# Kernel tuning notes

Hardware: AMD Instinct MI355X
Metric: run time of the kernel (lower is better)

Reference implementation:

```python
import jax, jax.numpy as jnp
import numpy as np

N_GRAM = 3
N_HEAD = 8


def setup_inputs() -> dict:
    key = jax.random.key(0)
    ks = jax.random.split(key, 8)
    V, E, H, H2, C, B, L = 50000, 512, 512, 512, 10, 64, 512
    def rn(k, shape, scale):
        return jax.random.normal(k, shape, jnp.float32) * jnp.float32(scale)
    return {
        "x": jax.random.randint(ks[0], (B, L), 0, V),
        "emb": rn(ks[1], (V, E), 0.02),
        "Wq": rn(ks[2], (H, E), 1.0 / np.sqrt(H)),
        "Wx": rn(ks[3], (E, 3 * H), 1.0 / np.sqrt(E)),
        "Wh": rn(ks[4], (H, 3 * H), 1.0 / np.sqrt(H)),
        "bx": jnp.zeros((3 * H,), jnp.float32),
        "bh": jnp.zeros((3 * H,), jnp.float32),
        "W1": rn(ks[5], (H, H2), 1.0 / np.sqrt(H)),
        "b1": jnp.zeros((H2,), jnp.float32),
        "W2": rn(ks[6], (H2, C), 1.0 / np.sqrt(H2)),
        "b2": jnp.zeros((C,), jnp.float32),
    }


def _gru_ngram_attn(xe, Wq, Wx, Wh, bx, bh):
    # xe: [B, L, E] embedded sequence
    B, L, E = xe.shape
    g, nh = N_GRAM, N_HEAD
    hd = E // nh
    H = Wh.shape[0]
    scale = jnp.float32(1.0 / np.sqrt(hd))
    xpad = jnp.pad(xe, ((0, 0), (g - 1, 0), (0, 0)))
    win = jnp.stack([xpad[:, i:i + L] for i in range(g)], axis=2)  # [B,L,g,E]
    win_t = jnp.transpose(win, (1, 0, 2, 3))  # [L,B,g,E] for scan
    h0 = jnp.zeros((B, H), xe.dtype)

    def step(h, w):
        # multi-head dot attention: query from prev hidden, keys/values = n-gram window
        q = (h @ Wq).reshape(B, nh, hd)          # [B,nh,hd]
        k = w.reshape(B, g, nh, hd)              # [B,g,nh,hd]
        scores = jnp.einsum('bnd,bgnd->bng', q, k) * scale
        a = jax.nn.softmax(scores, axis=-1)      # over window positions
        ctx = jnp.einsum('bng,bgnd->bnd', a, k).reshape(B, E)
        # GRU cell with attended context as input
        gx = ctx @ Wx + bx
        gh = h @ Wh + bh
        xr, xz, xn = jnp.split(gx, 3, axis=-1)
        hr, hz, hn = jnp.split(gh, 3, axis=-1)
        r = jax.nn.sigmoid(xr + hr)
        z = jax.nn.sigmoid(xz + hz)
        n = jnp.tanh(xn + r * hn)
        hnew = (1.0 - z) * n + z * h
        return hnew, hnew

    _, hs = jax.lax.scan(step, h0, win_t)  # [L,B,H]
    return hs


def reference(x, emb, Wq, Wx, Wh, bx, bh, W1, b1, W2, b2):
    xe = emb[x]  # [B,L,E]
    hs = _gru_ngram_attn(xe, Wq, Wx, Wh, bx, bh)  # [L,B,H]
    pooled = jax.nn.relu(hs.sum(axis=0))          # sum over seq, then relu
    out = pooled @ W1 + b1                        # fc1 path (H != embed not needed; H is GRU out)
    out = out @ W2 + b2                           # [B,C]
    return out
```

## Files before the change

kernel.cpp:

```cpp
#include <hip/hip_runtime.h>
#include <hip/hip_fp16.h>

typedef __attribute__((ext_vector_type(2))) _Float16 half2v;
typedef __attribute__((ext_vector_type(2))) __fp16   fp16x2;

#define SEQ     512
#define THREADS 512

#define WQ_OFF   0
#define WX_OFF   (64*512)
#define WH_OFF   (64*512 + 64*1536)
#define SYNC_OFF 3670016

__device__ inline unsigned int pack2f16(float a, float b) {
    fp16x2 p = __builtin_amdgcn_cvt_pkrtz(a, b);
    return __builtin_bit_cast(unsigned int, p);
}
__device__ inline float fdot2u(unsigned int a, unsigned int b, float acc) {
    return __builtin_amdgcn_fdot2(__builtin_bit_cast(half2v, a),
                                  __builtin_bit_cast(half2v, b), acc, false);
}
__device__ inline float dot4(uint4 h, uint4 w, float acc) {
    acc = fdot2u(h.x, w.x, acc); acc = fdot2u(h.y, w.y, acc);
    acc = fdot2u(h.z, w.z, acc); acc = fdot2u(h.w, w.w, acc);
    return acc;
}
__device__ inline float fsigmoid(float x) { return 1.f / (1.f + __expf(-x)); }
__device__ inline float ftanhf(float x) {
    float e = __expf(-2.f * fabsf(x));
    float t = (1.f - e) / (1.f + e);
    return copysignf(t, x);
}

__device__ inline void vmem_fence() { asm volatile("s_waitcnt vmcnt(0)" ::: "memory"); }
__device__ inline unsigned a_ld(unsigned* p) {
    return __hip_atomic_load(p, __ATOMIC_RELAXED, __HIP_MEMORY_SCOPE_AGENT);
}
__device__ inline void a_st(unsigned* p, unsigned v) {
    __hip_atomic_store(p, v, __ATOMIC_RELAXED, __HIP_MEMORY_SCOPE_AGENT);
}
__device__ inline float a_ldf(float* p) {
    return __hip_atomic_load(p, __ATOMIC_RELAXED, __HIP_MEMORY_SCOPE_AGENT);
}
__device__ inline void a_stf(float* p, float v) {
    __hip_atomic_store(p, v, __ATOMIC_RELAXED, __HIP_MEMORY_SCOPE_AGENT);
}

__global__ __launch_bounds__(256)
void pack_weights(const float* __restrict__ Wq,
                  const float* __restrict__ Wx,
                  const float* __restrict__ Wh,
                  uint4* __restrict__ ws) {
    int tid = blockIdx.x * blockDim.x + threadIdx.x;
    const float* src; uint4* dst; int C, idx;
    if (tid < 64 * 512)                  { src = Wq; dst = ws;          C = 512;  idx = tid; }
    else if (tid < 64 * 512 + 64 * 1536) { src = Wx; dst = ws + WX_OFF; C = 1536; idx = tid - 64 * 512; }
    else                                 { src = Wh; dst = ws + WH_OFF; C = 1536; idx = tid - (64 * 512 + 64 * 1536); }
    int m4 = idx / C;
    int c  = idx - m4 * C;
    const float* s = src + (size_t)(m4 * 8) * C + c;
    uint4 o;
    o.x = pack2f16(s[0 * (size_t)C], s[1 * (size_t)C]);
    o.y = pack2f16(s[2 * (size_t)C], s[3 * (size_t)C]);
    o.z = pack2f16(s[4 * (size_t)C], s[5 * (size_t)C]);
    o.w = pack2f16(s[6 * (size_t)C], s[7 * (size_t)C]);
    dst[idx] = o;
}

__global__ __launch_bounds__(THREADS)
void gru_scan(const int* __restrict__ xtok, const float* __restrict__ emb,
              const uint4* __restrict__ wsp, const float* __restrict__ bx,
              const float* __restrict__ bh, const float* __restrict__ W1,
              const float* __restrict__ b1, const float* __restrict__ W2,
              const float* __restrict__ b2, float* __restrict__ out)
{
    const int blk  = blockIdx.x;
    const int gid  = blk & 7;
    const int bid  = blk >> 3;
    const int tid  = threadIdx.x;
    const int lane = tid & 63;
    const int wid  = tid >> 6;
    const int colsub = lane & 7;
    const int bp     = (lane >> 3) & 3;
    const int chsub  = lane >> 5;

    char* sync = (char*)wsp + SYNC_OFF;
    unsigned int* flagS = (unsigned int*)sync;
    unsigned int* flagH = (unsigned int*)(sync + 1024);
    unsigned int* Hbuf  = (unsigned int*)(sync + 2048);
    float* Pbuf         = (float*)(sync + 133120);
    float* pooled_g     = (float*)(sync + 182272);
    float* fc1_g        = (float*)(sync + 313344);

    __shared__ uint4 lds_W [64][65];
    __shared__ uint4 lds_Wx[64][49];
    __shared__ uint4 lds_h [8][66];
    __shared__ uint4 lds_ctx[8][66];
    __shared__ float red[8][64][9];
    __shared__ float sum[64][9];
    __shared__ float a_lds[8][8][3];

    for (int i = tid; i < 64 * 64; i += THREADS) {
        int ch = i >> 6, cl = i & 63;
        uint4 v;
        if (cl < 16) v = wsp[WQ_OFF + ch * 512 + bid * 16 + cl];
        else { int g = (cl - 16) >> 4, c = (cl - 16) & 15;
               v = wsp[WH_OFF + ch * 1536 + g * 512 + bid * 16 + c]; }
        lds_W[ch][cl] = v;
    }
    for (int i = tid; i < 64 * 48; i += THREADS) {
        int ch = i / 48, cl = i - ch * 48;
        int g = cl >> 4, c = cl & 15;
        lds_Wx[ch][cl] = wsp[WX_OFF + ch * 1536 + g * 512 + bid * 16 + c];
    }

    float bxr = 0, bxz = 0, bxn = 0, bhr = 0, bhz = 0, bhn = 0;
    if (tid < 128) {
        int c = tid >> 3;
        int cg = bid * 16 + c;
        bxr = bx[cg]; bxz = bx[512 + cg]; bxn = bx[1024 + cg];
        bhr = bh[cg]; bhz = bh[512 + cg]; bhn = bh[1024 + cg];
    }
    float hprev = 0.f, pooledv = 0.f;
    __syncthreads();

    for (int t = 0; t < SEQ; ++t) {
        const int par = t & 1;

        const int b  = wid;
        const int gb = gid * 8 + b;
        int tk0 = (t >= 2) ? xtok[gb * SEQ + t - 2] : -1;
        int tk1 = (t >= 1) ? xtok[gb * SEQ + t - 1] : -1;
        int tk2 = xtok[gb * SEQ + t];
        float4 e0a = {0,0,0,0}, e0b = {0,0,0,0};
        float4 e1a = {0,0,0,0}, e1b = {0,0,0,0};
        float4 e2a, e2b;
        if (tk0 >= 0) { const float4* p = (const float4*)(emb + (size_t)tk0 * 512 + lane * 8); e0a = p[0]; e0b = p[1]; }
        if (tk1 >= 0) { const float4* p = (const float4*)(emb + (size_t)tk1 * 512 + lane * 8); e1a = p[0]; e1b = p[1]; }
        { const float4* p = (const float4*)(emb + (size_t)tk2 * 512 + lane * 8); e2a = p[0]; e2b = p[1]; }

        float winv[16];
        int b3 = 0, g3 = 0, trow = -1;
        if (wid == 0 && lane < 24) {
            b3 = lane / 3; g3 = lane - b3 * 3;
            trow = t - 2 + g3;
            int tok = (trow >= 0) ? xtok[(gid * 8 + b3) * SEQ + trow] : -1;
            if (tok >= 0) {
                const float* er = emb + (size_t)tok * 512 + bid * 16;
                #pragma unroll
                for (int d = 0; d < 16; ++d) winv[d] = er[d];
            } else {
                #pragma unroll
                for (int d = 0; d < 16; ++d) winv[d] = 0.f;
            }
        }

        if (wid == 0) {
            bool done = lane >= 32;
            while (!__all(done)) {
                if (!done) done = (a_ld(&flagH[gid * 32 + lane]) >= (unsigned)t);
                if (!__all(done)) __builtin_amdgcn_s_sleep(1);
            }
        }
        __syncthreads();

        {
            unsigned* hsrc = Hbuf + (size_t)(par ^ 1) * 16384;
            for (int i = tid; i < 8 * 64; i += THREADS) {
                int bb = i >> 6, ch = i & 63;
                unsigned* s = hsrc + (gid * 8 + bb) * 256 + ch * 4;
                uint4 v;
                v.x = a_ld(s); v.y = a_ld(s + 1); v.z = a_ld(s + 2); v.w = a_ld(s + 3);
                lds_h[bb][ch] = v;
            }
        }
        __syncthreads();

        {
            float aq0 = 0, aq1 = 0, aq2 = 0, aq3 = 0;
            int ch0 = wid * 8 + chsub * 4;
            #pragma unroll
            for (int i = 0; i < 4; ++i) {
                int ch = ch0 + i;
                uint4 h0 = lds_h[bp][ch], h1 = lds_h[bp + 4][ch];
                uint4 w0 = lds_W[ch][colsub], w1 = lds_W[ch][colsub + 8];
                aq0 = dot4(h0, w0, aq0); aq1 = dot4(h0, w1, aq1);
                aq2 = dot4(h1, w0, aq2); aq3 = dot4(h1, w1, aq3);
            }
            aq0 += __shfl_xor(aq0, 32); aq1 += __shfl_xor(aq1, 32);
            aq2 += __shfl_xor(aq2, 32); aq3 += __shfl_xor(aq3, 32);
            if (chsub == 0) {
                red[wid][colsub][bp]       = aq0; red[wid][colsub + 8][bp]     = aq1;
                red[wid][colsub][bp + 4]   = aq2; red[wid][colsub + 8][bp + 4] = aq3;
            }
        }
        __syncthreads();

        if (wid == 0 && lane < 24) {
            float s = 0.f;
            if (trow >= 0) {
                #pragma unroll
                for (int d = 0; d < 16; ++d) {
                    float q = red[0][d][b3];
                    #pragma unroll
                    for (int k = 1; k < 8; ++k) q += red[k][d][b3];
                    s += winv[d] * q;
                }
            }
            a_stf(&Pbuf[(size_t)((par * 8 + gid) * 32 + bid) * 24 + b3 * 3 + g3], s);
        }
        if (wid == 0) {
            vmem_fence();
            if (lane == 0) a_st(&flagS[gid * 32 + bid], (unsigned)(t + 1));
        }

        {
            float ag[12];
            #pragma unroll
            for (int i = 0; i < 12; ++i) ag[i] = 0.f;
            int ch0 = wid * 8 + chsub * 4;
            #pragma unroll
            for (int i = 0; i < 4; ++i) {
                int ch = ch0 + i;
                uint4 h0 = lds_h[bp][ch], h1 = lds_h[bp + 4][ch];
                #pragma unroll
                for (int j = 0; j < 6; ++j) {
                    uint4 w = lds_W[ch][16 + colsub + 8 * j];
                    ag[j]     = dot4(h0, w, ag[j]);
                    ag[6 + j] = dot4(h1, w, ag[6 + j]);
                }
            }
            #pragma unroll
            for (int i = 0; i < 12; ++i) ag[i] += __shfl_xor(ag[i], 32);
            if (chsub == 0) {
                #pragma unroll
                for (int j = 0; j < 6; ++j) {
                    red[wid][16 + colsub + 8 * j][bp]     = ag[j];
                    red[wid][16 + colsub + 8 * j][bp + 4] = ag[6 + j];
                }
            }
        }
        __syncthreads();

        if (tid >= 64 && tid < 448) {
            int idx = tid - 64;
            int col = 16 + (idx >> 3), bb = idx & 7;
            float s = red[0][col][bb];
            #pragma unroll
            for (int k = 1; k < 8; ++k) s += red[k][col][bb];
            sum[col][bb] = s;
        }
        if (wid == 0) {
            bool done = lane >= 32;
            while (!__all(done)) {
                if (!done) done = (a_ld(&flagS[gid * 32 + lane]) >= (unsigned)(t + 1));
                if (!__all(done)) __builtin_amdgcn_s_sleep(1);
            }
        }
        __syncthreads();

        if (tid < 64) {
            int bb = tid >> 3, n = tid & 7;
            float* pb = Pbuf + (size_t)(par * 8 + gid) * 32 * 24;
            float sc0 = 0, sc1 = 0, sc2 = 0;
            #pragma unroll
            for (int j = 0; j < 4; ++j) {
                float* pj = pb + (n * 4 + j) * 24 + bb * 3;
                sc0 += a_ldf(pj); sc1 += a_ldf(pj + 1); sc2 += a_ldf(pj + 2);
            }
            sc0 *= 0.125f; sc1 *= 0.125f; sc2 *= 0.125f;
            float mx = fmaxf(sc0, fmaxf(sc1, sc2));
            float e0 = __expf(sc0 - mx), e1 = __expf(sc1 - mx), e2 = __expf(sc2 - mx);
            float inv = 1.f / (e0 + e1 + e2);
            a_lds[bb][n][0] = e0 * inv; a_lds[bb][n][1] = e1 * inv; a_lds[bb][n][2] = e2 * inv;
        }
        __syncthreads();

        {
            int head = lane >> 3;
            float a0 = a_lds[b][head][0], a1 = a_lds[b][head][1], a2 = a_lds[b][head][2];
            float c0 = a0 * e0a.x + a1 * e1a.x + a2 * e2a.x;
            float c1 = a0 * e0a.y + a1 * e1a.y + a2 * e2a.y;
            float c2 = a0 * e0a.z + a1 * e1a.z + a2 * e2a.z;
            float c3 = a0 * e0a.w + a1 * e1a.w + a2 * e2a.w;
            float c4 = a0 * e0b.x + a1 * e1b.x + a2 * e2b.x;
            float c5 = a0 * e0b.y + a1 * e1b.y + a2 * e2b.y;
            float c6 = a0 * e0b.z + a1 * e1b.z + a2 * e2b.z;
            float c7 = a0 * e0b.w + a1 * e1b.w + a2 * e2b.w;
            uint4 pk;
            pk.x = pack2f16(c0, c1); pk.y = pack2f16(c2, c3);
            pk.z = pack2f16(c4, c5); pk.w = pack2f16(c6, c7);
            lds_ctx[b][lane] = pk;
        }
        __syncthreads();

        {
            float acx[12];
            #pragma unroll
            for (int i = 0; i < 12; ++i) acx[i] = 0.f;
            int ch0 = wid * 8 + chsub * 4;
            #pragma unroll
            for (int i = 0; i < 4; ++i) {
                int ch = ch0 + i;
                uint4 c0 = lds_ctx[bp][ch];
                uint4 c1 = lds_ctx[bp + 4][ch];
                #pragma unroll
                for (int j = 0; j < 6; ++j) {
                    uint4 w = lds_Wx[ch][colsub + 8 * j];
                    acx[j]     = dot4(c0, w, acx[j]);
                    acx[6 + j] = dot4(c1, w, acx[6 + j]);
                }
            }
            #pragma unroll
            for (int i = 0; i < 12; ++i) acx[i] += __shfl_xor(acx[i], 32);
            if (chsub == 0) {
                #pragma unroll
                for (int j = 0; j < 6; ++j) {
                    red[wid][colsub + 8 * j][bp]     = acx[j];
                    red[wid][colsub + 8 * j][bp + 4] = acx[6 + j];
                }
            }
        }
        __syncthreads();

        if (tid < 128) {
            int c = tid >> 3, bb = tid & 7;
            float gxr = bxr, gxz = bxz, gxn = bxn;
            #pragma unroll
            for (int k = 0; k < 8; ++k) {
                gxr += red[k][c][bb];
                gxz += red[k][16 + c][bb];
                gxn += red[k][32 + c][bb];
            }
            float ghr = sum[16 + c][bb] + bhr;
            float ghz = sum[32 + c][bb] + bhz;
            float ghn = sum[48 + c][bb] + bhn;
            float r = fsigmoid(gxr + ghr);
            float z = fsigmoid(gxz + ghz);
            float n = ftanhf(gxn + r * ghn);
            float hnew = (1.f - z) * n + z * hprev;
            hprev = hnew; pooledv += hnew;
            float hnext = __shfl_down(hnew, 8);
            if ((c & 1) == 0)
                a_st(&Hbuf[(size_t)par * 16384 + (gid * 8 + bb) * 256 + bid * 8 + (c >> 1)],
                     pack2f16(hnew, hnext));
        }
        vmem_fence();
        __syncthreads();
        if (tid == 0)
            a_st(&flagH[gid * 32 + bid], (unsigned)(t + 1));
    }

    float* stage = &red[0][0][0];
    if (tid < 128) {
        int c = tid >> 3, bb = tid & 7;
        a_stf(&pooled_g[(gid * 8 + bb) * 512 + bid * 16 + c], fmaxf(pooledv, 0.f));
    }
    vmem_fence();
    __syncthreads();
    if (tid == 0)
        a_st(&flagS[gid * 32 + bid], (unsigned)(SEQ + 1));
    if (wid == 0) {
        bool done = lane >= 32;
        while (!__all(done)) {
            if (!done) done = (a_ld(&flagS[gid * 32 + lane]) >= (unsigned)(SEQ + 1));
            if (!__all(done)) __builtin_amdgcn_s_sleep(1);
        }
    }
    __syncthreads();

    for (int i = tid; i < 8 * 512; i += THREADS) {
        int bb = i >> 9, k = i & 511;
        stage[bb * 512 + k] = a_ldf(&pooled_g[(gid * 8 + bb) * 512 + k]);
    }
    __syncthreads();

    if (tid < 128) {
        int c = tid >> 3, bb = tid & 7;
        int cg = bid * 16 + c;
        const float* pr = stage + bb * 512;
        float acc1 = b1[cg];
        for (int k = 0; k < 512; ++k) acc1 += pr[k] * W1[(size_t)k * 512 + cg];
        a_stf(&fc1_g[(gid * 8 + bb) * 512 + cg], acc1);
    }
    vmem_fence();
    __syncthreads();
    if (tid == 0)
        a_st(&flagH[gid * 32 + bid], (unsigned)(SEQ + 1));

    if (bid == 0) {
        if (wid == 0) {
            bool done = lane >= 32;
            while (!__all(done)) {
                if (!done) done = (a_ld(&flagH[gid * 32 + lane]) >= (unsigned)(SEQ + 1));
                if (!__all(done)) __builtin_amdgcn_s_sleep(1);
            }
        }
        __syncthreads();
        for (int i = tid; i < 8 * 512; i += THREADS) {
            int bb = i >> 9, k = i & 511;
            stage[bb * 512 + k] = a_ldf(&fc1_g[(gid * 8 + bb) * 512 + k]);
        }
        __syncthreads();
        if (tid < 80) {
            int bb = tid / 10, cls = tid - bb * 10;
            const float* fr = stage + bb * 512;
            float a2 = b2[cls];
            for (int k = 0; k < 512; ++k) a2 += fr[k] * W2[k * 10 + cls];
            out[(gid * 8 + bb) * 10 + cls] = a2;
        }
    }
}

extern "C" void kernel_launch(void* const* d_in, const int* in_sizes, int n_in,
                              void* d_out, int out_size, void* d_ws, size_t ws_size,
                              hipStream_t stream) {
    const int*   x   = (const int*)d_in[0];
    const float* emb = (const float*)d_in[1];
    const float* Wq  = (const float*)d_in[2];
    const float* Wx  = (const float*)d_in[3];
    const float* Wh  = (const float*)d_in[4];
    const float* bx  = (const float*)d_in[5];
    const float* bh  = (const float*)d_in[6];
    const float* W1  = (const float*)d_in[7];
    const float* b1  = (const float*)d_in[8];
    const float* W2  = (const float*)d_in[9];
    const float* b2  = (const float*)d_in[10];
    uint4* wsp = (uint4*)d_ws;
    float* outp = (float*)d_out;

    hipLaunchKernelGGL(pack_weights, dim3(896), dim3(256), 0, stream, Wq, Wx, Wh, wsp);
    hipMemsetAsync((char*)d_ws + SYNC_OFF, 0, 133120, stream);

    void* args[] = { (void*)&x, (void*)&emb, (void*)&wsp, (void*)&bx, (void*)&bh,
                     (void*)&W1, (void*)&b1, (void*)&W2, (void*)&b2, (void*)&outp };
    hipError_t e = hipLaunchCooperativeKernel((void*)gru_scan, dim3(256), dim3(THREADS),
                                              args, 0, stream);
    if (e != hipSuccess) {
        hipLaunchKernelGGL(gru_scan, dim3(256), dim3(THREADS), 0, stream,
                           x, emb, wsp, bx, bh, W1, b1, W2, b2, outp);
    }
}
```

Before: 4.268 ms.

## Reassociate attention scores as h·(Wq·k) to remove per-step cross-block sync

Attention scores are now computed as h_t dotted with a precomputed per-block projection of the window embeddings through Wq (kap). Each block writes partial score contributions from its new hidden slice, and the next step sums them, so the intra-step flagS barrier and the separate Wq matvec phase go away. Embedding rows are also carried in registers as a rolling window with a one-step prefetch instead of being reloaded three times per step. In exchange there is extra per-step projection work, a larger Pbuf with a wider memset, and more LDS use.

```diff
diff --git a/kernel.cpp b/kernel.cpp
--- a/kernel.cpp
+++ b/kernel.cpp
@@ -7,9 +7,9 @@
 #define SEQ     512
 #define THREADS 512
 
-#define WQ_OFF   0
-#define WX_OFF   (64*512)
-#define WH_OFF   (64*512 + 64*1536)
+#define WX_OFF   0
+#define WH_OFF   98304
+#define WQR_OFF  196608
 #define SYNC_OFF 3670016
 
 __device__ inline unsigned int pack2f16(float a, float b) {
@@ -31,7 +31,6 @@
     float t = (1.f - e) / (1.f + e);
     return copysignf(t, x);
 }
-
 __device__ inline void vmem_fence() { asm volatile("s_waitcnt vmcnt(0)" ::: "memory"); }
 __device__ inline unsigned a_ld(unsigned* p) {
     return __hip_atomic_load(p, __ATOMIC_RELAXED, __HIP_MEMORY_SCOPE_AGENT);
@@ -52,19 +51,28 @@
                   const float* __restrict__ Wh,
                   uint4* __restrict__ ws) {
     int tid = blockIdx.x * blockDim.x + threadIdx.x;
-    const float* src; uint4* dst; int C, idx;
-    if (tid < 64 * 512)                  { src = Wq; dst = ws;          C = 512;  idx = tid; }
-    else if (tid < 64 * 512 + 64 * 1536) { src = Wx; dst = ws + WX_OFF; C = 1536; idx = tid - 64 * 512; }
-    else                                 { src = Wh; dst = ws + WH_OFF; C = 1536; idx = tid - (64 * 512 + 64 * 1536); }
-    int m4 = idx / C;
-    int c  = idx - m4 * C;
-    const float* s = src + (size_t)(m4 * 8) * C + c;
-    uint4 o;
-    o.x = pack2f16(s[0 * (size_t)C], s[1 * (size_t)C]);
-    o.y = pack2f16(s[2 * (size_t)C], s[3 * (size_t)C]);
-    o.z = pack2f16(s[4 * (size_t)C], s[5 * (size_t)C]);
-    o.w = pack2f16(s[6 * (size_t)C], s[7 * (size_t)C]);
-    dst[idx] = o;
+    if (tid < 196608) {
+        const float* src; uint4* dst; int idx;
+        if (tid < 98304) { src = Wx; dst = ws + WX_OFF; idx = tid; }
+        else             { src = Wh; dst = ws + WH_OFF; idx = tid - 98304; }
+        int m4 = idx / 1536;
+        int c  = idx - m4 * 1536;
+        const float* s = src + (size_t)(m4 * 8) * 1536 + c;
+        uint4 o;
+        o.x = pack2f16(s[0 * 1536], s[1 * 1536]);
+        o.y = pack2f16(s[2 * 1536], s[3 * 1536]);
+        o.z = pack2f16(s[4 * 1536], s[5 * 1536]);
+        o.w = pack2f16(s[6 * 1536], s[7 * 1536]);
+        dst[idx] = o;
+    } else {
+        int idx = tid - 196608;
+        int m = idx >> 6, q = idx & 63;
+        const float* s = Wq + (size_t)m * 512 + q * 8;
+        uint4 o;
+        o.x = pack2f16(s[0], s[1]); o.y = pack2f16(s[2], s[3]);
+        o.z = pack2f16(s[4], s[5]); o.w = pack2f16(s[6], s[7]);
+        ws[WQR_OFF + idx] = o;
+    }
 }
 
 __global__ __launch_bounds__(THREADS)
@@ -84,34 +92,35 @@
     const int bp     = (lane >> 3) & 3;
     const int chsub  = lane >> 5;
 
-    char* sync = (char*)wsp + SYNC_OFF;
-    unsigned int* flagS = (unsigned int*)sync;
-    unsigned int* flagH = (unsigned int*)(sync + 1024);
-    unsigned int* Hbuf  = (unsigned int*)(sync + 2048);
-    float* Pbuf         = (float*)(sync + 133120);
-    float* pooled_g     = (float*)(sync + 182272);
-    float* fc1_g        = (float*)(sync + 313344);
-
-    __shared__ uint4 lds_W [64][65];
-    __shared__ uint4 lds_Wx[64][49];
-    __shared__ uint4 lds_h [8][66];
+    char* syncb = (char*)wsp + SYNC_OFF;
+    unsigned* flagH = (unsigned*)syncb;
+    unsigned* flagS = (unsigned*)(syncb + 1024);
+    unsigned* Hbuf  = (unsigned*)(syncb + 2048);
+    float* Pbuf     = (float*)(syncb + 133120);
+    float* pooled_g = (float*)(syncb + 526336);
+    float* fc1_g    = (float*)(syncb + 657408);
+
+    __shared__ uint4 lds_Wh[64][48];
+    __shared__ uint4 lds_Wx[64][48];
+    __shared__ uint4 lds_Wqr[16][64];
+    __shared__ uint4 lds_h4[8][66];
     __shared__ uint4 lds_ctx[8][66];
-    __shared__ float red[8][64][9];
-    __shared__ float sum[64][9];
+    __shared__ float red[8][48][9];
+    __shared__ float sum[48][9];
+    __shared__ float kap[16][8][24];
+    __shared__ float hsl[8][17];
+    __shared__ float scmem[8][24];
     __shared__ float a_lds[8][8][3];
 
-    for (int i = tid; i < 64 * 64; i += THREADS) {
-        int ch = i >> 6, cl = i & 63;
-        uint4 v;
-        if (cl < 16) v = wsp[WQ_OFF + ch * 512 + bid * 16 + cl];
-        else { int g = (cl - 16) >> 4, c = (cl - 16) & 15;
-               v = wsp[WH_OFF + ch * 1536 + g * 512 + bid * 16 + c]; }
-        lds_W[ch][cl] = v;
-    }
     for (int i = tid; i < 64 * 48; i += THREADS) {
         int ch = i / 48, cl = i - ch * 48;
         int g = cl >> 4, c = cl & 15;
+        lds_Wh[ch][cl] = wsp[WH_OFF + ch * 1536 + g * 512 + bid * 16 + c];
         lds_Wx[ch][cl] = wsp[WX_OFF + ch * 1536 + g * 512 + bid * 16 + c];
+    }
+    for (int i = tid; i < 16 * 64; i += THREADS) {
+        int m = i >> 6, q = i & 63;
+        lds_Wqr[m][q] = wsp[WQR_OFF + (bid * 16 + m) * 64 + q];
     }
 
     float bxr = 0, bxz = 0, bxn = 0, bhr = 0, bhz = 0, bhn = 0;
@@ -121,37 +130,61 @@
         bxr = bx[cg]; bxz = bx[512 + cg]; bxn = bx[1024 + cg];
         bhr = bh[cg]; bhz = bh[512 + cg]; bhn = bh[1024 + cg];
     }
+
+    const int b  = wid;
+    const int gb = gid * 8 + b;
+    float4 r0a = {0,0,0,0}, r0b = {0,0,0,0};
+    float4 r1a = {0,0,0,0}, r1b = {0,0,0,0};
+    float4 r2a, r2b;
+    { int tk = xtok[gb * SEQ];
+      const float4* p = (const float4*)(emb + (size_t)tk * 512 + lane * 8);
+      r2a = p[0]; r2b = p[1]; }
+    unsigned pk1[4] = {0, 0, 0, 0};
+    unsigned pk2[4];
+    pk2[0] = pack2f16(r2a.x, r2a.y); pk2[1] = pack2f16(r2a.z, r2a.w);
+    pk2[2] = pack2f16(r2b.x, r2b.y); pk2[3] = pack2f16(r2b.z, r2b.w);
+
     float hprev = 0.f, pooledv = 0.f;
     __syncthreads();
 
     for (int t = 0; t < SEQ; ++t) {
         const int par = t & 1;
 
-        const int b  = wid;
-        const int gb = gid * 8 + b;
-        int tk0 = (t >= 2) ? xtok[gb * SEQ + t - 2] : -1;
-        int tk1 = (t >= 1) ? xtok[gb * SEQ + t - 1] : -1;
-        int tk2 = xtok[gb * SEQ + t];
-        float4 e0a = {0,0,0,0}, e0b = {0,0,0,0};
-        float4 e1a = {0,0,0,0}, e1b = {0,0,0,0};
-        float4 e2a, e2b;
-        if (tk0 >= 0) { const float4* p = (const float4*)(emb + (size_t)tk0 * 512 + lane * 8); e0a = p[0]; e0b = p[1]; }
-        if (tk1 >= 0) { const float4* p = (const float4*)(emb + (size_t)tk1 * 512 + lane * 8); e1a = p[0]; e1b = p[1]; }
-        { const float4* p = (const float4*)(emb + (size_t)tk2 * 512 + lane * 8); e2a = p[0]; e2b = p[1]; }
-
-        float winv[16];
-        int b3 = 0, g3 = 0, trow = -1;
-        if (wid == 0 && lane < 24) {
-            b3 = lane / 3; g3 = lane - b3 * 3;
-            trow = t - 2 + g3;
-            int tok = (trow >= 0) ? xtok[(gid * 8 + b3) * SEQ + trow] : -1;
-            if (tok >= 0) {
-                const float* er = emb + (size_t)tok * 512 + bid * 16;
-                #pragma unroll
-                for (int d = 0; d < 16; ++d) winv[d] = er[d];
-            } else {
-                #pragma unroll
-                for (int d = 0; d < 16; ++d) winv[d] = 0.f;
+        float4 r3a = {0,0,0,0}, r3b = {0,0,0,0};
+        if (t + 1 < SEQ) {
+            int tk = xtok[gb * SEQ + t + 1];
+            const float4* p = (const float4*)(emb + (size_t)tk * 512 + lane * 8);
+            r3a = p[0]; r3b = p[1];
+        }
+        unsigned pk3[4];
+        pk3[0] = pack2f16(r3a.x, r3a.y); pk3[1] = pack2f16(r3a.z, r3a.w);
+        pk3[2] = pack2f16(r3b.x, r3b.y); pk3[3] = pack2f16(r3b.z, r3b.w);
+
+        {
+            const int s  = lane & 7;
+            const int n3 = (lane >> 3) * 3;
+            #pragma unroll
+            for (int m = 0; m < 16; ++m) {
+                uint4 wq = lds_Wqr[m][lane];
+                float p0 = fdot2u(pk1[0], wq.x, 0.f);
+                p0 = fdot2u(pk1[1], wq.y, p0);
+                p0 = fdot2u(pk1[2], wq.z, p0);
+                p0 = fdot2u(pk1[3], wq.w, p0);
+                float p1 = fdot2u(pk2[0], wq.x, 0.f);
+                p1 = fdot2u(pk2[1], wq.y, p1);
+                p1 = fdot2u(pk2[2], wq.z, p1);
+                p1 = fdot2u(pk2[3], wq.w, p1);
+                float p2 = fdot2u(pk3[0], wq.x, 0.f);
+                p2 = fdot2u(pk3[1], wq.y, p2);
+                p2 = fdot2u(pk3[2], wq.z, p2);
+                p2 = fdot2u(pk3[3], wq.w, p2);
+                p0 += __shfl_xor(p0, 1); p1 += __shfl_xor(p1, 1); p2 += __shfl_xor(p2, 1);
+                p0 += __shfl_xor(p0, 2); p1 += __shfl_xor(p1, 2); p2 += __shfl_xor(p2, 2);
+                p0 += __shfl_xor(p0, 4); p1 += __shfl_xor(p1, 4); p2 += __shfl_xor(p2, 4);
+                if (s == (m & 7)) {
+                    float* kp = &kap[m][b][n3];
+                    kp[0] = p0; kp[1] = p1; kp[2] = p2;
+                }
             }
         }
 
@@ -165,67 +198,33 @@
         __syncthreads();
 
         {
-            unsigned* hsrc = Hbuf + (size_t)(par ^ 1) * 16384;
-            for (int i = tid; i < 8 * 64; i += THREADS) {
-                int bb = i >> 6, ch = i & 63;
-                unsigned* s = hsrc + (gid * 8 + bb) * 256 + ch * 4;
-                uint4 v;
-                v.x = a_ld(s); v.y = a_ld(s + 1); v.z = a_ld(s + 2); v.w = a_ld(s + 3);
-                lds_h[bb][ch] = v;
-            }
+            int bb = tid >> 6, ch = tid & 63;
+            unsigned* s = Hbuf + (size_t)(par ^ 1) * 16384 + (gid * 8 + bb) * 256 + ch * 4;
+            uint4 v;
+            v.x = a_ld(s); v.y = a_ld(s + 1); v.z = a_ld(s + 2); v.w = a_ld(s + 3);
+            lds_h4[bb][ch] = v;
+        }
+        if (tid < 192) {
+            float* pb = Pbuf + (size_t)(par ^ 1) * 8 * 6144 + gid * 6144;
+            float sc = 0.f;
+            #pragma unroll
+            for (int k = 0; k < 32; ++k) sc += a_ldf(pb + k * 192 + tid);
+            scmem[tid / 24][tid % 24] = sc;
         }
         __syncthreads();
 
         {
-            float aq0 = 0, aq1 = 0, aq2 = 0, aq3 = 0;
+            float ag[12];
+            #pragma unroll
+            for (int i = 0; i < 12; ++i) ag[i] = 0.f;
             int ch0 = wid * 8 + chsub * 4;
             #pragma unroll
             for (int i = 0; i < 4; ++i) {
                 int ch = ch0 + i;
-                uint4 h0 = lds_h[bp][ch], h1 = lds_h[bp + 4][ch];
-                uint4 w0 = lds_W[ch][colsub], w1 = lds_W[ch][colsub + 8];
-                aq0 = dot4(h0, w0, aq0); aq1 = dot4(h0, w1, aq1);
-                aq2 = dot4(h1, w0, aq2); aq3 = dot4(h1, w1, aq3);
-            }
-            aq0 += __shfl_xor(aq0, 32); aq1 += __shfl_xor(aq1, 32);
-            aq2 += __shfl_xor(aq2, 32); aq3 += __shfl_xor(aq3, 32);
-            if (chsub == 0) {
-                red[wid][colsub][bp]       = aq0; red[wid][colsub + 8][bp]     = aq1;
-                red[wid][colsub][bp + 4]   = aq2; red[wid][colsub + 8][bp + 4] = aq3;
-            }
-        }
-        __syncthreads();
-
-        if (wid == 0 && lane < 24) {
-            float s = 0.f;
-            if (trow >= 0) {
-                #pragma unroll
-                for (int d = 0; d < 16; ++d) {
-                    float q = red[0][d][b3];
-                    #pragma unroll
-                    for (int k = 1; k < 8; ++k) q += red[k][d][b3];
-                    s += winv[d] * q;
-                }
-            }
-            a_stf(&Pbuf[(size_t)((par * 8 + gid) * 32 + bid) * 24 + b3 * 3 + g3], s);
-        }
-        if (wid == 0) {
-            vmem_fence();
-            if (lane == 0) a_st(&flagS[gid * 32 + bid], (unsigned)(t + 1));
-        }
-
-        {
-            float ag[12];
-            #pragma unroll
-            for (int i = 0; i < 12; ++i) ag[i] = 0.f;
-            int ch0 = wid * 8 + chsub * 4;
-            #pragma unroll
-            for (int i = 0; i < 4; ++i) {
-                int ch = ch0 + i;
-                uint4 h0 = lds_h[bp][ch], h1 = lds_h[bp + 4][ch];
+                uint4 h0 = lds_h4[bp][ch], h1 = lds_h4[bp + 4][ch];
                 #pragma unroll
                 for (int j = 0; j < 6; ++j) {
-                    uint4 w = lds_W[ch][16 + colsub + 8 * j];
+                    uint4 w = lds_Wh[ch][colsub + 8 * j];
                     ag[j]     = dot4(h0, w, ag[j]);
                     ag[6 + j] = dot4(h1, w, ag[6 + j]);
                 }
@@ -235,42 +234,18 @@
             if (chsub == 0) {
                 #pragma unroll
                 for (int j = 0; j < 6; ++j) {
-                    red[wid][16 + colsub + 8 * j][bp]     = ag[j];
-                    red[wid][16 + colsub + 8 * j][bp + 4] = ag[6 + j];
+                    red[wid][colsub + 8 * j][bp]     = ag[j];
+                    red[wid][colsub + 8 * j][bp + 4] = ag[6 + j];
                 }
             }
         }
-        __syncthreads();
-
-        if (tid >= 64 && tid < 448) {
-            int idx = tid - 64;
-            int col = 16 + (idx >> 3), bb = idx & 7;
-            float s = red[0][col][bb];
-            #pragma unroll
-            for (int k = 1; k < 8; ++k) s += red[k][col][bb];
-            sum[col][bb] = s;
-        }
-        if (wid == 0) {
-            bool done = lane >= 32;
-            while (!__all(done)) {
-                if (!done) done = (a_ld(&flagS[gid * 32 + lane]) >= (unsigned)(t + 1));
-                if (!__all(done)) __builtin_amdgcn_s_sleep(1);
-            }
-        }
-        __syncthreads();
-
         if (tid < 64) {
             int bb = tid >> 3, n = tid & 7;
-            float* pb = Pbuf + (size_t)(par * 8 + gid) * 32 * 24;
-            float sc0 = 0, sc1 = 0, sc2 = 0;
-            #pragma unroll
-            for (int j = 0; j < 4; ++j) {
-                float* pj = pb + (n * 4 + j) * 24 + bb * 3;
-                sc0 += a_ldf(pj); sc1 += a_ldf(pj + 1); sc2 += a_ldf(pj + 2);
-            }
-            sc0 *= 0.125f; sc1 *= 0.125f; sc2 *= 0.125f;
-            float mx = fmaxf(sc0, fmaxf(sc1, sc2));
-            float e0 = __expf(sc0 - mx), e1 = __expf(sc1 - mx), e2 = __expf(sc2 - mx);
+            float s0 = scmem[bb][n * 3 + 0] * 0.125f;
+            float s1 = scmem[bb][n * 3 + 1] * 0.125f;
+            float s2 = scmem[bb][n * 3 + 2] * 0.125f;
+            float mx = fmaxf(s0, fmaxf(s1, s2));
+            float e0 = __expf(s0 - mx), e1 = __expf(s1 - mx), e2 = __expf(s2 - mx);
             float inv = 1.f / (e0 + e1 + e2);
             a_lds[bb][n][0] = e0 * inv; a_lds[bb][n][1] = e1 * inv; a_lds[bb][n][2] = e2 * inv;
         }
@@ -279,18 +254,25 @@
         {
             int head = lane >> 3;
             float a0 = a_lds[b][head][0], a1 = a_lds[b][head][1], a2 = a_lds[b][head][2];
-            float c0 = a0 * e0a.x + a1 * e1a.x + a2 * e2a.x;
-            float c1 = a0 * e0a.y + a1 * e1a.y + a2 * e2a.y;
-            float c2 = a0 * e0a.z + a1 * e1a.z + a2 * e2a.z;
-            float c3 = a0 * e0a.w + a1 * e1a.w + a2 * e2a.w;
-            float c4 = a0 * e0b.x + a1 * e1b.x + a2 * e2b.x;
-            float c5 = a0 * e0b.y + a1 * e1b.y + a2 * e2b.y;
-            float c6 = a0 * e0b.z + a1 * e1b.z + a2 * e2b.z;
-            float c7 = a0 * e0b.w + a1 * e1b.w + a2 * e2b.w;
+            float c0 = a0 * r0a.x + a1 * r1a.x + a2 * r2a.x;
+            float c1 = a0 * r0a.y + a1 * r1a.y + a2 * r2a.y;
+            float c2 = a0 * r0a.z + a1 * r1a.z + a2 * r2a.z;
+            float c3 = a0 * r0a.w + a1 * r1a.w + a2 * r2a.w;
+            float c4 = a0 * r0b.x + a1 * r1b.x + a2 * r2b.x;
+            float c5 = a0 * r0b.y + a1 * r1b.y + a2 * r2b.y;
+            float c6 = a0 * r0b.z + a1 * r1b.z + a2 * r2b.z;
+            float c7 = a0 * r0b.w + a1 * r1b.w + a2 * r2b.w;
             uint4 pk;
             pk.x = pack2f16(c0, c1); pk.y = pack2f16(c2, c3);
             pk.z = pack2f16(c4, c5); pk.w = pack2f16(c6, c7);
             lds_ctx[b][lane] = pk;
+        }
+        if (tid < 384) {
+            int col = tid >> 3, bb = tid & 7;
+            float s = red[0][col][bb];
+            #pragma unroll
+            for (int k = 1; k < 8; ++k) s += red[k][col][bb];
+            sum[col][bb] = s;
         }
         __syncthreads();
 
@@ -332,34 +314,46 @@
                 gxz += red[k][16 + c][bb];
                 gxn += red[k][32 + c][bb];
             }
-            float ghr = sum[16 + c][bb] + bhr;
-            float ghz = sum[32 + c][bb] + bhz;
-            float ghn = sum[48 + c][bb] + bhn;
+            float ghr = sum[c][bb] + bhr;
+            float ghz = sum[16 + c][bb] + bhz;
+            float ghn = sum[32 + c][bb] + bhn;
             float r = fsigmoid(gxr + ghr);
             float z = fsigmoid(gxz + ghz);
             float n = ftanhf(gxn + r * ghn);
             float hnew = (1.f - z) * n + z * hprev;
             hprev = hnew; pooledv += hnew;
+            hsl[bb][c] = hnew;
             float hnext = __shfl_down(hnew, 8);
             if ((c & 1) == 0)
                 a_st(&Hbuf[(size_t)par * 16384 + (gid * 8 + bb) * 256 + bid * 8 + (c >> 1)],
                      pack2f16(hnew, hnext));
         }
+        __syncthreads();
+
+        if (tid < 192) {
+            int bb = tid / 24, r = tid % 24;
+            float p = 0.f;
+            #pragma unroll
+            for (int m = 0; m < 16; ++m) p += hsl[bb][m] * kap[m][bb][r];
+            a_stf(Pbuf + (size_t)par * 8 * 6144 + gid * 6144 + bid * 192 + tid, p);
+        }
         vmem_fence();
         __syncthreads();
-        if (tid == 0)
-            a_st(&flagH[gid * 32 + bid], (unsigned)(t + 1));
-    }
-
-    float* stage = &red[0][0][0];
+        if (tid == 0) a_st(&flagH[gid * 32 + bid], (unsigned)(t + 1));
+
+        r0a = r1a; r0b = r1b; r1a = r2a; r1b = r2b; r2a = r3a; r2b = r3b;
+        pk1[0] = pk2[0]; pk1[1] = pk2[1]; pk1[2] = pk2[2]; pk1[3] = pk2[3];
+        pk2[0] = pk3[0]; pk2[1] = pk3[1]; pk2[2] = pk3[2]; pk2[3] = pk3[3];
+    }
+
+    float* stage = (float*)&lds_Wh[0][0];
     if (tid < 128) {
         int c = tid >> 3, bb = tid & 7;
         a_stf(&pooled_g[(gid * 8 + bb) * 512 + bid * 16 + c], fmaxf(pooledv, 0.f));
     }
     vmem_fence();
     __syncthreads();
-    if (tid == 0)
-        a_st(&flagS[gid * 32 + bid], (unsigned)(SEQ + 1));
+    if (tid == 0) a_st(&flagS[gid * 32 + bid], (unsigned)(SEQ + 1));
     if (wid == 0) {
         bool done = lane >= 32;
         while (!__all(done)) {
@@ -385,14 +379,13 @@
     }
     vmem_fence();
     __syncthreads();
-    if (tid == 0)
-        a_st(&flagH[gid * 32 + bid], (unsigned)(SEQ + 1));
+    if (tid == 0) a_st(&flagH[gid * 32 + bid], (unsigned)(SEQ + 2));
 
     if (bid == 0) {
         if (wid == 0) {
             bool done = lane >= 32;
             while (!__all(done)) {
-                if (!done) done = (a_ld(&flagH[gid * 32 + lane]) >= (unsigned)(SEQ + 1));
+                if (!done) done = (a_ld(&flagH[gid * 32 + lane]) >= (unsigned)(SEQ + 2));
                 if (!__all(done)) __builtin_amdgcn_s_sleep(1);
             }
         }
@@ -430,7 +423,7 @@
     float* outp = (float*)d_out;
 
     hipLaunchKernelGGL(pack_weights, dim3(896), dim3(256), 0, stream, Wq, Wx, Wh, wsp);
-    hipMemsetAsync((char*)d_ws + SYNC_OFF, 0, 133120, stream);
+    hipMemsetAsync((char*)d_ws + SYNC_OFF, 0, 526336, stream);
 
     void* args[] = { (void*)&x, (void*)&emb, (void*)&wsp, (void*)&bx, (void*)&bh,
                      (void*)&W1, (void*)&b1, (void*)&W2, (void*)&b2, (void*)&outp };
```

After: 4.956 ms. 16.1% more time.

## Precompute per-token Wx projections and mix them with attention weights after softmax

Applied to the files above, without the earlier changes.

Uses linearity: ctx@Wx equals the attention-weighted sum of each window token's embedding projected by Wx. Each token's per-head Wx projection is computed once, ahead of the h-dependent wait, and kept in a 3-slot fp16 ring in LDS. After the softmax, gx is formed as a small weighted sum instead of a full context matmul, which removes one matmul and several barriers from the serial critical path. The Wh gate matmul now overlaps with wave 0's cross-block softmax sync. The trade-off is extra fp16 rounding of the projected values, more complex LDS indexing, and one wave doing double Wh work.

```diff
diff --git a/kernel.cpp b/kernel.cpp
--- a/kernel.cpp
+++ b/kernel.cpp
@@ -8,8 +8,8 @@
 #define THREADS 512
 
 #define WQ_OFF   0
-#define WX_OFF   (64*512)
-#define WH_OFF   (64*512 + 64*1536)
+#define WX_OFF   32768
+#define WH_OFF   131072
 #define SYNC_OFF 3670016
 
 __device__ inline unsigned int pack2f16(float a, float b) {
@@ -31,7 +31,6 @@
     float t = (1.f - e) / (1.f + e);
     return copysignf(t, x);
 }
-
 __device__ inline void vmem_fence() { asm volatile("s_waitcnt vmcnt(0)" ::: "memory"); }
 __device__ inline unsigned a_ld(unsigned* p) {
     return __hip_atomic_load(p, __ATOMIC_RELAXED, __HIP_MEMORY_SCOPE_AGENT);
@@ -84,21 +83,21 @@
     const int bp     = (lane >> 3) & 3;
     const int chsub  = lane >> 5;
 
-    char* sync = (char*)wsp + SYNC_OFF;
-    unsigned int* flagS = (unsigned int*)sync;
-    unsigned int* flagH = (unsigned int*)(sync + 1024);
-    unsigned int* Hbuf  = (unsigned int*)(sync + 2048);
-    float* Pbuf         = (float*)(sync + 133120);
-    float* pooled_g     = (float*)(sync + 182272);
-    float* fc1_g        = (float*)(sync + 313344);
+    char* syncb = (char*)wsp + SYNC_OFF;
+    unsigned* flagH = (unsigned*)syncb;
+    unsigned* flagS = (unsigned*)(syncb + 1024);
+    unsigned* Hbuf  = (unsigned*)(syncb + 2048);
+    float* Pbuf     = (float*)(syncb + 133120);
+    float* pooled_g = (float*)(syncb + 182272);
+    float* fc1_g    = (float*)(syncb + 313344);
 
     __shared__ uint4 lds_W [64][65];
     __shared__ uint4 lds_Wx[64][49];
-    __shared__ uint4 lds_h [8][66];
-    __shared__ uint4 lds_ctx[8][66];
-    __shared__ float red[8][64][9];
-    __shared__ float sum[64][9];
-    __shared__ float a_lds[8][8][3];
+    __shared__ uint4 lds_h4[8][65];
+    __shared__ unsigned u_pk[3][8][48][4];
+    __shared__ float redQf[1152];
+    __shared__ float redH[8][48][9];
+    __shared__ float a_all[8][8][3];
 
     for (int i = tid; i < 64 * 64; i += THREADS) {
         int ch = i >> 6, cl = i & 63;
@@ -116,28 +115,34 @@
 
     float bxr = 0, bxz = 0, bxn = 0, bhr = 0, bhz = 0, bhn = 0;
     if (tid < 128) {
-        int c = tid >> 3;
-        int cg = bid * 16 + c;
+        int c = tid >> 3, cg = bid * 16 + c;
         bxr = bx[cg]; bxz = bx[512 + cg]; bxn = bx[1024 + cg];
         bhr = bh[cg]; bhz = bh[512 + cg]; bhn = bh[1024 + cg];
     }
+
+    const int gb = gid * 8 + wid;
+    {
+        int tk = xtok[gb * SEQ];
+        const float4* p = (const float4*)(emb + (size_t)tk * 512 + lane * 8);
+        float4 ra = p[0], rb = p[1];
+        uint4 pk;
+        pk.x = pack2f16(ra.x, ra.y); pk.y = pack2f16(ra.z, ra.w);
+        pk.z = pack2f16(rb.x, rb.y); pk.w = pack2f16(rb.z, rb.w);
+        lds_h4[wid][lane] = pk;
+        unsigned* up = &u_pk[0][0][0][0];
+        for (int i = tid; i < 3072; i += THREADS) up[1536 + i] = 0u;
+    }
     float hprev = 0.f, pooledv = 0.f;
     __syncthreads();
 
     for (int t = 0; t < SEQ; ++t) {
         const int par = t & 1;
-
-        const int b  = wid;
-        const int gb = gid * 8 + b;
-        int tk0 = (t >= 2) ? xtok[gb * SEQ + t - 2] : -1;
-        int tk1 = (t >= 1) ? xtok[gb * SEQ + t - 1] : -1;
-        int tk2 = xtok[gb * SEQ + t];
-        float4 e0a = {0,0,0,0}, e0b = {0,0,0,0};
-        float4 e1a = {0,0,0,0}, e1b = {0,0,0,0};
-        float4 e2a, e2b;
-        if (tk0 >= 0) { const float4* p = (const float4*)(emb + (size_t)tk0 * 512 + lane * 8); e0a = p[0]; e0b = p[1]; }
-        if (tk1 >= 0) { const float4* p = (const float4*)(emb + (size_t)tk1 * 512 + lane * 8); e1a = p[0]; e1b = p[1]; }
-        { const float4* p = (const float4*)(emb + (size_t)tk2 * 512 + lane * 8); e2a = p[0]; e2b = p[1]; }
+        const int slot = t % 3;
+
+        int tnext = (t + 1 < SEQ) ? (t + 1) : t;
+        int tkn = xtok[gb * SEQ + tnext];
+        const float4* pn = (const float4*)(emb + (size_t)tkn * 512 + lane * 8);
+        float4 r3a = pn[0], r3b = pn[1];
 
         float winv[16];
         int b3 = 0, g3 = 0, trow = -1;
@@ -155,6 +160,31 @@
             }
         }
 
+        {
+            float acu[12];
+            #pragma unroll
+            for (int i = 0; i < 12; ++i) acu[i] = 0.f;
+            int ch0 = wid * 8 + chsub * 4;
+            #pragma unroll
+            for (int i = 0; i < 4; ++i) {
+                int ch = ch0 + i;
+                uint4 c0 = lds_h4[bp][ch], c1 = lds_h4[bp + 4][ch];
+                #pragma unroll
+                for (int j = 0; j < 6; ++j) {
+                    uint4 w = lds_Wx[ch][colsub + 8 * j];
+                    acu[j]     = dot4(c0, w, acu[j]);
+                    acu[6 + j] = dot4(c1, w, acu[6 + j]);
+                }
+            }
+            #pragma unroll
+            for (int i = 0; i < 12; ++i) acu[i] += __shfl_xor(acu[i], 32);
+            if (chsub == 0) {
+                #pragma unroll
+                for (int j = 0; j < 6; ++j)
+                    u_pk[slot][wid][colsub + 8 * j][bp] = pack2f16(acu[j], acu[6 + j]);
+            }
+        }
+
         if (wid == 0) {
             bool done = lane >= 32;
             while (!__all(done)) {
@@ -165,14 +195,11 @@
         __syncthreads();
 
         {
-            unsigned* hsrc = Hbuf + (size_t)(par ^ 1) * 16384;
-            for (int i = tid; i < 8 * 64; i += THREADS) {
-                int bb = i >> 6, ch = i & 63;
-                unsigned* s = hsrc + (gid * 8 + bb) * 256 + ch * 4;
-                uint4 v;
-                v.x = a_ld(s); v.y = a_ld(s + 1); v.z = a_ld(s + 2); v.w = a_ld(s + 3);
-                lds_h[bb][ch] = v;
-            }
+            int bb = tid >> 6, c4 = tid & 63;
+            unsigned* s = Hbuf + (size_t)(par ^ 1) * 16384 + (gid * 8 + bb) * 256 + c4 * 4;
+            uint4 v;
+            v.x = a_ld(s); v.y = a_ld(s + 1); v.z = a_ld(s + 2); v.w = a_ld(s + 3);
+            lds_h4[bb][c4] = v;
         }
         __syncthreads();
 
@@ -182,7 +209,7 @@
             #pragma unroll
             for (int i = 0; i < 4; ++i) {
                 int ch = ch0 + i;
-                uint4 h0 = lds_h[bp][ch], h1 = lds_h[bp + 4][ch];
+                uint4 h0 = lds_h4[bp][ch], h1 = lds_h4[bp + 4][ch];
                 uint4 w0 = lds_W[ch][colsub], w1 = lds_W[ch][colsub + 8];
                 aq0 = dot4(h0, w0, aq0); aq1 = dot4(h0, w1, aq1);
                 aq2 = dot4(h1, w0, aq2); aq3 = dot4(h1, w1, aq3);
@@ -190,151 +217,119 @@
             aq0 += __shfl_xor(aq0, 32); aq1 += __shfl_xor(aq1, 32);
             aq2 += __shfl_xor(aq2, 32); aq3 += __shfl_xor(aq3, 32);
             if (chsub == 0) {
-                red[wid][colsub][bp]       = aq0; red[wid][colsub + 8][bp]     = aq1;
-                red[wid][colsub][bp + 4]   = aq2; red[wid][colsub + 8][bp + 4] = aq3;
-            }
-        }
-        __syncthreads();
-
-        if (wid == 0 && lane < 24) {
-            float s = 0.f;
-            if (trow >= 0) {
-                #pragma unroll
-                for (int d = 0; d < 16; ++d) {
-                    float q = red[0][d][b3];
+                redQf[(wid * 16 + colsub) * 9 + bp]         = aq0;
+                redQf[(wid * 16 + colsub + 8) * 9 + bp]     = aq1;
+                redQf[(wid * 16 + colsub) * 9 + bp + 4]     = aq2;
+                redQf[(wid * 16 + colsub + 8) * 9 + bp + 4] = aq3;
+            }
+        }
+        __syncthreads();
+
+        if (wid == 0) {
+            if (lane < 24) {
+                float s = 0.f;
+                if (trow >= 0) {
                     #pragma unroll
-                    for (int k = 1; k < 8; ++k) q += red[k][d][b3];
-                    s += winv[d] * q;
-                }
-            }
-            a_stf(&Pbuf[(size_t)((par * 8 + gid) * 32 + bid) * 24 + b3 * 3 + g3], s);
-        }
-        if (wid == 0) {
+                    for (int d = 0; d < 16; ++d) {
+                        float q = redQf[d * 9 + b3];
+                        #pragma unroll
+                        for (int k = 1; k < 8; ++k) q += redQf[(k * 16 + d) * 9 + b3];
+                        s += winv[d] * q;
+                    }
+                }
+                a_stf(&Pbuf[(size_t)((par * 8 + gid) * 32 + bid) * 24 + b3 * 3 + g3], s);
+            }
             vmem_fence();
             if (lane == 0) a_st(&flagS[gid * 32 + bid], (unsigned)(t + 1));
-        }
-
-        {
-            float ag[12];
-            #pragma unroll
-            for (int i = 0; i < 12; ++i) ag[i] = 0.f;
-            int ch0 = wid * 8 + chsub * 4;
-            #pragma unroll
-            for (int i = 0; i < 4; ++i) {
-                int ch = ch0 + i;
-                uint4 h0 = lds_h[bp][ch], h1 = lds_h[bp + 4][ch];
-                #pragma unroll
-                for (int j = 0; j < 6; ++j) {
-                    uint4 w = lds_W[ch][16 + colsub + 8 * j];
-                    ag[j]     = dot4(h0, w, ag[j]);
-                    ag[6 + j] = dot4(h1, w, ag[6 + j]);
-                }
-            }
-            #pragma unroll
-            for (int i = 0; i < 12; ++i) ag[i] += __shfl_xor(ag[i], 32);
-            if (chsub == 0) {
-                #pragma unroll
-                for (int j = 0; j < 6; ++j) {
-                    red[wid][16 + colsub + 8 * j][bp]     = ag[j];
-                    red[wid][16 + colsub + 8 * j][bp + 4] = ag[6 + j];
-                }
-            }
-        }
-        __syncthreads();
-
-        if (tid >= 64 && tid < 448) {
-            int idx = tid - 64;
-            int col = 16 + (idx >> 3), bb = idx & 7;
-            float s = red[0][col][bb];
-            #pragma unroll
-            for (int k = 1; k < 8; ++k) s += red[k][col][bb];
-            sum[col][bb] = s;
-        }
-        if (wid == 0) {
             bool done = lane >= 32;
             while (!__all(done)) {
                 if (!done) done = (a_ld(&flagS[gid * 32 + lane]) >= (unsigned)(t + 1));
                 if (!__all(done)) __builtin_amdgcn_s_sleep(1);
             }
-        }
-        __syncthreads();
-
-        if (tid < 64) {
-            int bb = tid >> 3, n = tid & 7;
-            float* pb = Pbuf + (size_t)(par * 8 + gid) * 32 * 24;
-            float sc0 = 0, sc1 = 0, sc2 = 0;
-            #pragma unroll
-            for (int j = 0; j < 4; ++j) {
-                float* pj = pb + (n * 4 + j) * 24 + bb * 3;
-                sc0 += a_ldf(pj); sc1 += a_ldf(pj + 1); sc2 += a_ldf(pj + 2);
-            }
-            sc0 *= 0.125f; sc1 *= 0.125f; sc2 *= 0.125f;
-            float mx = fmaxf(sc0, fmaxf(sc1, sc2));
-            float e0 = __expf(sc0 - mx), e1 = __expf(sc1 - mx), e2 = __expf(sc2 - mx);
-            float inv = 1.f / (e0 + e1 + e2);
-            a_lds[bb][n][0] = e0 * inv; a_lds[bb][n][1] = e1 * inv; a_lds[bb][n][2] = e2 * inv;
-        }
-        __syncthreads();
-
+            {
+                int bb = lane >> 3, n = lane & 7;
+                float* pb = Pbuf + (size_t)(par * 8 + gid) * 32 * 24;
+                float sc0 = 0, sc1 = 0, sc2 = 0;
+                #pragma unroll
+                for (int j = 0; j < 4; ++j) {
+                    float* pj = pb + (n * 4 + j) * 24 + bb * 3;
+                    sc0 += a_ldf(pj); sc1 += a_ldf(pj + 1); sc2 += a_ldf(pj + 2);
+                }
+                sc0 *= 0.125f; sc1 *= 0.125f; sc2 *= 0.125f;
+                float mx = fmaxf(sc0, fmaxf(sc1, sc2));
+                float e0 = __expf(sc0 - mx), e1 = __expf(sc1 - mx), e2 = __expf(sc2 - mx);
+                float inv = 1.f / (e0 + e1 + e2);
+                a_all[bb][n][0] = e0 * inv; a_all[bb][n][1] = e1 * inv; a_all[bb][n][2] = e2 * inv;
+            }
+        } else {
+            #pragma unroll 1
+            for (int rep = 0; rep < 2; ++rep) {
+                int k = (rep == 0) ? wid : 0;
+                if (rep == 1 && wid != 7) break;
+                float ag[12];
+                #pragma unroll
+                for (int i = 0; i < 12; ++i) ag[i] = 0.f;
+                int ch0 = k * 8 + chsub * 4;
+                #pragma unroll
+                for (int i = 0; i < 4; ++i) {
+                    int ch = ch0 + i;
+                    uint4 h0 = lds_h4[bp][ch], h1 = lds_h4[bp + 4][ch];
+                    #pragma unroll
+                    for (int j = 0; j < 6; ++j) {
+                        uint4 w = lds_W[ch][16 + colsub + 8 * j];
+                        ag[j]     = dot4(h0, w, ag[j]);
+                        ag[6 + j] = dot4(h1, w, ag[6 + j]);
+                    }
+                }
+                #pragma unroll
+                for (int i = 0; i < 12; ++i) ag[i] += __shfl_xor(ag[i], 32);
+                if (chsub == 0) {
+                    #pragma unroll
+                    for (int j = 0; j < 6; ++j) {
+                        redH[k][colsub + 8 * j][bp]     = ag[j];
+                        redH[k][colsub + 8 * j][bp + 4] = ag[6 + j];
+                    }
+                }
+            }
+        }
+        __syncthreads();
+
+        if (tid >= 64 && tid < 448) {
+            int idx = tid - 64;
+            int col = idx >> 3, bb = idx & 7;
+            float ghs = redH[0][col][bb];
+            #pragma unroll
+            for (int k = 1; k < 8; ++k) ghs += redH[k][col][bb];
+            float gxs = 0.f;
+            int half = bb >> 2, bq = bb & 3;
+            #pragma unroll
+            for (int g = 0; g < 3; ++g) {
+                int sg = (t + 1 + g) % 3;
+                #pragma unroll
+                for (int k = 0; k < 8; ++k) {
+                    fp16x2 uv = __builtin_bit_cast(fp16x2, u_pk[sg][k][col][bq]);
+                    gxs += a_all[bb][k][g] * (float)uv[half];
+                }
+            }
+            redQf[col * 8 + bb]       = ghs;
+            redQf[384 + col * 8 + bb] = gxs;
+        }
         {
-            int head = lane >> 3;
-            float a0 = a_lds[b][head][0], a1 = a_lds[b][head][1], a2 = a_lds[b][head][2];
-            float c0 = a0 * e0a.x + a1 * e1a.x + a2 * e2a.x;
-            float c1 = a0 * e0a.y + a1 * e1a.y + a2 * e2a.y;
-            float c2 = a0 * e0a.z + a1 * e1a.z + a2 * e2a.z;
-            float c3 = a0 * e0a.w + a1 * e1a.w + a2 * e2a.w;
-            float c4 = a0 * e0b.x + a1 * e1b.x + a2 * e2b.x;
-            float c5 = a0 * e0b.y + a1 * e1b.y + a2 * e2b.y;
-            float c6 = a0 * e0b.z + a1 * e1b.z + a2 * e2b.z;
-            float c7 = a0 * e0b.w + a1 * e1b.w + a2 * e2b.w;
             uint4 pk;
-            pk.x = pack2f16(c0, c1); pk.y = pack2f16(c2, c3);
-            pk.z = pack2f16(c4, c5); pk.w = pack2f16(c6, c7);
-            lds_ctx[b][lane] = pk;
-        }
-        __syncthreads();
-
-        {
-            float acx[12];
-            #pragma unroll
-            for (int i = 0; i < 12; ++i) acx[i] = 0.f;
-            int ch0 = wid * 8 + chsub * 4;
-            #pragma unroll
-            for (int i = 0; i < 4; ++i) {
-                int ch = ch0 + i;
-                uint4 c0 = lds_ctx[bp][ch];
-                uint4 c1 = lds_ctx[bp + 4][ch];
-                #pragma unroll
-                for (int j = 0; j < 6; ++j) {
-                    uint4 w = lds_Wx[ch][colsub + 8 * j];
-                    acx[j]     = dot4(c0, w, acx[j]);
-                    acx[6 + j] = dot4(c1, w, acx[6 + j]);
-                }
-            }
-            #pragma unroll
-            for (int i = 0; i < 12; ++i) acx[i] += __shfl_xor(acx[i], 32);
-            if (chsub == 0) {
-                #pragma unroll
-                for (int j = 0; j < 6; ++j) {
-                    red[wid][colsub + 8 * j][bp]     = acx[j];
-                    red[wid][colsub + 8 * j][bp + 4] = acx[6 + j];
-                }
-            }
+            pk.x = pack2f16(r3a.x, r3a.y); pk.y = pack2f16(r3a.z, r3a.w);
+            pk.z = pack2f16(r3b.x, r3b.y); pk.w = pack2f16(r3b.z, r3b.w);
+            lds_h4[wid][lane] = pk;
         }
         __syncthreads();
 
         if (tid < 128) {
             int c = tid >> 3, bb = tid & 7;
-            float gxr = bxr, gxz = bxz, gxn = bxn;
-            #pragma unroll
-            for (int k = 0; k < 8; ++k) {
-                gxr += red[k][c][bb];
-                gxz += red[k][16 + c][bb];
-                gxn += red[k][32 + c][bb];
-            }
-            float ghr = sum[16 + c][bb] + bhr;
-            float ghz = sum[32 + c][bb] + bhz;
-            float ghn = sum[48 + c][bb] + bhn;
+            float ghr = redQf[c * 8 + bb]        + bhr;
+            float ghz = redQf[(16 + c) * 8 + bb] + bhz;
+            float ghn = redQf[(32 + c) * 8 + bb] + bhn;
+            float gxr = redQf[384 + c * 8 + bb]        + bxr;
+            float gxz = redQf[384 + (16 + c) * 8 + bb] + bxz;
+            float gxn = redQf[384 + (32 + c) * 8 + bb] + bxn;
             float r = fsigmoid(gxr + ghr);
             float z = fsigmoid(gxz + ghz);
             float n = ftanhf(gxn + r * ghn);
@@ -347,19 +342,17 @@
         }
         vmem_fence();
         __syncthreads();
-        if (tid == 0)
-            a_st(&flagH[gid * 32 + bid], (unsigned)(t + 1));
-    }
-
-    float* stage = &red[0][0][0];
+        if (tid == 0) a_st(&flagH[gid * 32 + bid], (unsigned)(t + 1));
+    }
+
+    float* stage = (float*)&lds_W[0][0];
     if (tid < 128) {
         int c = tid >> 3, bb = tid & 7;
         a_stf(&pooled_g[(gid * 8 + bb) * 512 + bid * 16 + c], fmaxf(pooledv, 0.f));
     }
     vmem_fence();
     __syncthreads();
-    if (tid == 0)
-        a_st(&flagS[gid * 32 + bid], (unsigned)(SEQ + 1));
+    if (tid == 0) a_st(&flagS[gid * 32 + bid], (unsigned)(SEQ + 1));
     if (wid == 0) {
         bool done = lane >= 32;
         while (!__all(done)) {
@@ -385,14 +378,13 @@
     }
     vmem_fence();
     __syncthreads();
-    if (tid == 0)
-        a_st(&flagH[gid * 32 + bid], (unsigned)(SEQ + 1));
+    if (tid == 0) a_st(&flagH[gid * 32 + bid], (unsigned)(SEQ + 2));
 
     if (bid == 0) {
         if (wid == 0) {
             bool done = lane >= 32;
             while (!__all(done)) {
-                if (!done) done = (a_ld(&flagH[gid * 32 + lane]) >= (unsigned)(SEQ + 1));
+                if (!done) done = (a_ld(&flagH[gid * 32 + lane]) >= (unsigned)(SEQ + 2));
                 if (!__all(done)) __builtin_amdgcn_s_sleep(1);
             }
         }
@@ -430,7 +422,7 @@
     float* outp = (float*)d_out;
 
     hipLaunchKernelGGL(pack_weights, dim3(896), dim3(256), 0, stream, Wq, Wx, Wh, wsp);
-    hipMemsetAsync((char*)d_ws + SYNC_OFF, 0, 133120, stream);
+    hipMemsetAsync((char*)d_ws + SYNC_OFF, 0, 182272, stream);
 
     void* args[] = { (void*)&x, (void*)&emb, (void*)&wsp, (void*)&bx, (void*)&bh,
                      (void*)&W1, (void*)&b1, (void*)&W2, (void*)&b2, (void*)&outp };
```

After: 3.621 ms, median of 2. 15.2% less time.
